# Kernel optimization log

Measured on AMD Instinct MI355X. Metric: run time of the kernel, lower is better.

The kernel has to match this reference:

```python
import jax, jax.numpy as jnp
import numpy as np
from math import sqrt

B, S, E, H = 2, 2048, 768, 12
DH = E // H
W = 256            # one-sided attention window (attention_window=512)
G = 16             # number of global tokens (positions 0..G-1 in every batch row)
PAD = 128          # last PAD tokens per row are padding (masked)
FF = 3072          # SwiGLU intermediate size
NEG = -1e9
EPS = 1e-5


def _ln(x, g, b):
    m = jnp.mean(x, axis=-1, keepdims=True)
    v = jnp.var(x, axis=-1, keepdims=True)
    return (x - m) * jax.lax.rsqrt(v + EPS) * g + b


def _rope(x, t):
    # x: [B,H,S,DH]; t: [B,S] float 'set positions'
    half = DH // 2
    inv_freq = 1.0 / (10000.0 ** (jnp.arange(half, dtype=jnp.float32) / half))
    ang = t[:, None, :, None] * inv_freq            # [B,1,S,half]
    cos, sin = jnp.cos(ang), jnp.sin(ang)
    x1, x2 = x[..., :half], x[..., half:]
    return jnp.concatenate([x1 * cos - x2 * sin, x2 * cos + x1 * sin], axis=-1)


def _heads(x):  # [B,S,E] -> [B,H,S,DH]
    return x.reshape(B, S, H, DH).transpose(0, 2, 1, 3)


def _chunk3(x):
    # [B,H,S,D] -> [B,H,C,3W,D]: for query chunk c, keys from chunks c-1,c,c+1 (zero padded)
    b, h, s, d = x.shape
    c = s // W
    xp = jnp.pad(x, ((0, 0), (0, 0), (W, W), (0, 0))).reshape(b, h, c + 2, W, d)
    return jnp.concatenate([xp[:, :, :-2], xp[:, :, 1:-1], xp[:, :, 2:]], axis=3)


def _forward(x, attention_mask, global_attention_mask,
             Wq, bq, Wk, bk, Wv, bv, Wqg, bqg, Wkg, bkg, Wvg, bvg,
             ln0_g, ln0_b, ln1_g, ln1_b, W1, W3, W2):
    C = S // W
    merged = attention_mask * (global_attention_mask + 1)   # 0 masked, 1 local, 2 global
    is_masked = merged == 0
    is_global = merged == 2
    remove = merged != 1   # keys removed from windowed attention (masked or global)

    q = _heads(x @ Wq + bq) / sqrt(DH)
    k = _heads(x @ Wk + bk)
    v = _heads(x @ Wv + bv)

    # RoPE over 'set positions': (~is_index_masked) * cumsum(is_index_global_attn)
    t = jnp.where(is_masked, 0, jnp.cumsum(is_global.astype(jnp.int32), axis=1)).astype(jnp.float32)
    q = _rope(q, t)
    k = _rope(k, t)

    # --- sliding-window (banded) scores: band[b,h,i,d] = q_i . k_{i+d-W} ---
    qc = q.reshape(B, H, C, W, DH)
    k3 = _chunk3(k)
    s3 = jnp.einsum('bhcpd,bhcqd->bhcpq', qc, k3)                     # [B,H,C,W,3W]
    didx = jnp.arange(W)[:, None] + jnp.arange(2 * W + 1)[None, :]    # [W,2W+1]
    band = jnp.take_along_axis(s3, didx[None, None, None], axis=-1)   # [B,H,C,W,2W+1]

    # mask removed keys / out-of-range positions inside the band
    rmp = jnp.pad(remove, ((0, 0), (W, W)), constant_values=True).reshape(B, C + 2, W)
    rm3 = jnp.concatenate([rmp[:, :-2], rmp[:, 1:-1], rmp[:, 2:]], axis=2)  # [B,C,3W]
    band_rm = jnp.take_along_axis(jnp.broadcast_to(rm3[:, :, None, :], (B, C, W, 3 * W)),
                                  didx[None, None], axis=-1)                # [B,C,W,2W+1]
    band = jnp.where(band_rm[:, None], NEG, band).reshape(B, H, S, 2 * W + 1)

    # --- global-key columns (keys taken from the RoPE'd local key vectors) ---
    sg = jnp.einsum('bhid,bhgd->bhig', q, k[:, :, :G])                # [B,H,S,G]

    scores = jnp.concatenate([sg, band], axis=-1)                     # [B,H,S,G+2W+1]
    probs = jax.nn.softmax(scores.astype(jnp.float32), axis=-1).astype(x.dtype)
    probs = jnp.where(is_masked[:, None, :, None], 0.0, probs)

    # --- probs @ value: global columns + band ---
    out = jnp.einsum('bhig,bhgd->bhid', probs[..., :G], v[:, :, :G])
    pl = probs[..., G:].reshape(B, H, C, W, 2 * W + 1)
    rows = jnp.broadcast_to(jnp.arange(W)[:, None], (W, 2 * W + 1))
    p3 = jnp.zeros((B, H, C, W, 3 * W), probs.dtype).at[:, :, :, rows, didx].set(pl)
    v3 = _chunk3(v)
    out = out + jnp.einsum('bhcpq,bhcqd->bhcpd', p3, v3).reshape(B, H, S, DH)
    attn = out.transpose(0, 2, 1, 3).reshape(B, S, E)

    # --- full attention for global tokens (separate global projections, no RoPE) ---
    gq = _heads(x @ Wqg + bqg)[:, :, :G] / sqrt(DH)                   # [B,H,G,DH]
    gk = _heads(x @ Wkg + bkg)
    gv = _heads(x @ Wvg + bvg)
    gs = jnp.einsum('bhgd,bhjd->bhgj', gq, gk)                        # [B,H,G,S]
    gs = jnp.where(is_masked[:, None, None, :], NEG, gs)
    gp = jax.nn.softmax(gs.astype(jnp.float32), axis=-1).astype(x.dtype)
    gout = jnp.einsum('bhgj,bhjd->bhgd', gp, gv).transpose(0, 2, 1, 3).reshape(B, G, E)
    attn = attn.at[:, :G].set(gout)

    # residual + post-LN, SwiGLU FFN, residual + post-LN (dropout = eval mode)
    h0 = _ln(x + attn, ln0_g, ln0_b)
    ffn = (jax.nn.silu(h0 @ W1) * (h0 @ W3)) @ W2
    return _ln(h0 + ffn, ln1_g, ln1_b)


def setup_inputs():
    key = jax.random.key(0)
    ks = jax.random.split(key, 12)
    x = jax.random.normal(ks[0], (B, S, E), jnp.float32)
    attention_mask = jnp.ones((B, S), jnp.int32).at[:, S - PAD:].set(0)
    global_attention_mask = jnp.zeros((B, S), jnp.int32).at[:, :G].set(1)
    sd = 0.02
    def w(k, shape):
        return jax.random.normal(k, shape, jnp.float32) * sd
    return dict(
        x=x, attention_mask=attention_mask, global_attention_mask=global_attention_mask,
        Wq=w(ks[1], (E, E)), bq=jnp.zeros((E,), jnp.float32),
        Wk=w(ks[2], (E, E)), bk=jnp.zeros((E,), jnp.float32),
        Wv=w(ks[3], (E, E)), bv=jnp.zeros((E,), jnp.float32),
        Wqg=w(ks[4], (E, E)), bqg=jnp.zeros((E,), jnp.float32),
        Wkg=w(ks[5], (E, E)), bkg=jnp.zeros((E,), jnp.float32),
        Wvg=w(ks[6], (E, E)), bvg=jnp.zeros((E,), jnp.float32),
        ln0_g=jnp.ones((E,), jnp.float32), ln0_b=jnp.zeros((E,), jnp.float32),
        ln1_g=jnp.ones((E,), jnp.float32), ln1_b=jnp.zeros((E,), jnp.float32),
        W1=w(ks[7], (E, FF)), W3=w(ks[8], (E, FF)), W2=w(ks[9], (FF, E)))


def reference(x, attention_mask, global_attention_mask, Wq, bq, Wk, bk, Wv, bv,
              Wqg, bqg, Wkg, bkg, Wvg, bvg, ln0_g, ln0_b, ln1_g, ln1_b, W1, W3, W2):
    return _forward(x, attention_mask, global_attention_mask,
                    Wq, bq, Wk, bk, Wv, bv, Wqg, bqg, Wkg, bkg, Wvg, bvg,
                    ln0_g, ln0_b, ln1_g, ln1_b, W1, W3, W2)
```

## Files before the change

kernel.cpp:

```cpp
#include <hip/hip_runtime.h>


#define BB_ 2
#define SS 2048
#define EE 768
#define HH 12
#define DHH 64
#define GG 16
#define FFN 3072
#define MM (BB_*SS)

typedef __bf16 bf16_t;
typedef __bf16 bf16x8_t __attribute__((ext_vector_type(8)));
typedef float f32x4_t __attribute__((ext_vector_type(4)));

__device__ inline void gload16(const void* g, void* l) {
  __builtin_amdgcn_global_load_lds((const __attribute__((address_space(1))) void*)g,
                                   (__attribute__((address_space(3))) void*)l, 16, 0, 0);
}

__global__ __launch_bounds__(64) void detect_kernel(const unsigned int* __restrict__ w,
                                                    int* __restrict__ flag) {
  int cnt = 0;
  for (int i = threadIdx.x; i < 1024; i += 64) {
    unsigned e = (w[i] >> 7) & 0xFF;
    cnt += (e >= 100 && e <= 144) ? 1 : 0;
  }
  for (int off = 32; off; off >>= 1) cnt += __shfl_xor(cnt, off);
  if (threadIdx.x == 0) flag[0] = (cnt > 512) ? 1 : 0;
}

struct CanonP { const void* src[11]; bf16_t* dst[11]; };

__global__ __launch_bounds__(256) void canon_kernel(CanonP P, const int* __restrict__ flag) {
  constexpr int ns[11] = {3145728, 768,768,768,768,768,768, 768,768,768,768};
  int idx4 = (blockIdx.x*256 + threadIdx.x)*4;
  const bool isb = flag[0] != 0;
  int off = 0, seg = -1, loc = 0;
  #pragma unroll
  for (int i=0;i<11;i++) {
    if (seg < 0 && idx4 < off + ns[i]) { seg = i; loc = idx4 - off; }
    off += ns[i];
  }
  if (seg < 0) return;
  const void* s = P.src[seg];
  bf16_t* d = P.dst[seg];
  if (isb) {
    *(uint2*)&d[loc] = *(const uint2*)((const unsigned short*)s + loc);
  } else {
    float4 v = *(const float4*)((const float*)s + loc);
    d[loc+0] = (bf16_t)v.x; d[loc+1] = (bf16_t)v.y;
    d[loc+2] = (bf16_t)v.z; d[loc+3] = (bf16_t)v.w;
  }
}

struct TP6 { const void* s[6]; bf16_t* d[6]; };

__global__ __launch_bounds__(256) void trans_kernel(TP6 P, int R, int C,
                                                    const int* __restrict__ flag) {
  const int z = blockIdx.z;
  const void* src = P.s[z]; bf16_t* dst = P.d[z];
  const bool isb = flag[0] != 0;
  __shared__ bf16_t tile[32][33];
  int tx = threadIdx.x & 31, ty = threadIdx.x >> 5;
  int r0 = blockIdx.y*32, c0 = blockIdx.x*32;
  #pragma unroll
  for (int i=0;i<4;i++) {
    int rr = ty + i*8;
    size_t si = (size_t)(r0+rr)*C + c0 + tx;
    tile[rr][tx] = isb ? ((const bf16_t*)src)[si] : (bf16_t)((const float*)src)[si];
  }
  __syncthreads();
  #pragma unroll
  for (int i=0;i<4;i++) {
    int cc = ty + i*8;
    dst[(size_t)(c0+cc)*R + r0 + tx] = tile[tx][cc];
  }
}

__global__ __launch_bounds__(256) void zero_kernel(float* __restrict__ p, int n) {
  int i = blockIdx.x*256 + threadIdx.x;
  if (i < n) p[i] = 0.f;
}

__global__ __launch_bounds__(256) void flags_kernel(const int* __restrict__ am,
                                                    const int* __restrict__ gm,
                                                    float* __restrict__ tpos,
                                                    int* __restrict__ flags) {
  int b = blockIdx.x;
  int t = threadIdx.x;
  int lane = t & 63, wv = t >> 6;
  int base = b*SS + t*8;
  int mg[8]; int isg[8]; int loc = 0;
  for (int i=0;i<8;i++) {
    int a = am[base+i], g = gm[base+i];
    int merged = a*(g+1);
    mg[i] = merged;
    isg[i] = (merged==2) ? 1 : 0;
    loc += isg[i];
  }
  int x = loc;
  for (int off=1; off<64; off<<=1) {
    int y = __shfl_up(x, off);
    if (lane >= off) x += y;
  }
  __shared__ int wtot[4];
  if (lane==63) wtot[wv] = x;
  __syncthreads();
  int prev = 0;
  for (int w=0; w<wv; w++) prev += wtot[w];
  int run = prev + x - loc;
  for (int i=0;i<8;i++) {
    run += isg[i];
    int masked = (mg[i]==0) ? 1 : 0;
    int glob   = (mg[i]==2) ? 1 : 0;
    int rem    = (mg[i]!=1) ? 1 : 0;
    tpos[base+i]  = masked ? 0.f : (float)run;
    flags[base+i] = masked | (glob<<1) | (rem<<2);
  }
}

__device__ inline void gemm128_core(const bf16_t* __restrict__ A,
                                    const bf16_t* __restrict__ BT,
                                    int ldA, int ldB, int kbeg, int kend,
                                    int m0, int n0,
                                    bf16_t* As, bf16_t* Bs,
                                    f32x4_t (&acc)[4][4]) {
  const int t = threadIdx.x;
  const int lane = t & 63, wv = t >> 6;
  const int l15 = lane & 15, quad = lane >> 4;
  const int wr = (wv >> 1) << 6, wc = (wv & 1) << 6;
  const int rsub = lane >> 3, pch = lane & 7;
  const int sch = pch ^ rsub;
  const size_t abase = (size_t)(m0 + wv*32 + rsub)*ldA + sch*8;
  const size_t bbase = (size_t)(n0 + wv*32 + rsub)*ldB + sch*8;
  const int sx = l15 & 7;
  bf16_t* lA = As + (wv*32)*64;
  bf16_t* lB = Bs + (wv*32)*64;
  for (int k0 = kbeg; k0 < kend; k0 += 64) {
    __syncthreads();
    #pragma unroll
    for (int j=0;j<4;j++) {
      gload16(A + abase + (size_t)(j*8)*ldA + k0, lA + j*8*64);
      gload16(BT + bbase + (size_t)(j*8)*ldB + k0, lB + j*8*64);
    }
    __syncthreads();
    #pragma unroll
    for (int c=0;c<2;c++) {
      bf16x8_t af[4], bfr[4];
      #pragma unroll
      for (int a=0;a<4;a++)
        af[a] = *(const bf16x8_t*)&As[(wr + a*16 + l15)*64 + ((c*4+quad)^sx)*8];
      #pragma unroll
      for (int b=0;b<4;b++)
        bfr[b] = *(const bf16x8_t*)&Bs[(wc + b*16 + l15)*64 + ((c*4+quad)^sx)*8];
      #pragma unroll
      for (int a=0;a<4;a++)
        #pragma unroll
        for (int b=0;b<4;b++)
          acc[a][b] = __builtin_amdgcn_mfma_f32_16x16x32_bf16(af[a], bfr[b], acc[a][b], 0,0,0);
    }
  }
}

struct ProjParams {
  const bf16_t* W[5];
  const bf16_t* Bi[5];
  bf16_t* O[5];
};

__global__ __launch_bounds__(256) void proj_kernel(const bf16_t* __restrict__ x,
                                                   ProjParams P,
                                                   const float* __restrict__ tpos) {
  const int m0 = blockIdx.x*128, n0 = blockIdx.y*128;
  const int z  = blockIdx.z;
  __shared__ bf16_t As[128*64];
  __shared__ bf16_t Bs[128*64];
  f32x4_t acc[4][4];
  #pragma unroll
  for (int a=0;a<4;a++)
    #pragma unroll
    for (int b=0;b<4;b++) acc[a][b] = (f32x4_t){0.f,0.f,0.f,0.f};
  gemm128_core(x, P.W[z], EE, EE, 0, EE, m0, n0, As, Bs, acc);

  const int t = threadIdx.x;
  const int lane = t & 63, wv = t >> 6;
  const int l15 = lane & 15, quad = lane >> 4;
  const int wr = (wv >> 1) << 6, wc = (wv & 1) << 6;
  const float scale = (z==0) ? 0.125f : 1.f;
  const bool rope = (z<2);
  const int h = (n0 + wc) >> 6;
  bf16_t* Oz = P.O[z];
  const bf16_t* Bz = P.Bi[z];
  float bvals[4];
  #pragma unroll
  for (int b=0;b<4;b++) bvals[b] = (float)Bz[h*64 + b*16 + l15];
  #pragma unroll
  for (int a=0;a<4;a++) {
    #pragma unroll
    for (int r=0;r<4;r++) {
      int row = m0 + wr + a*16 + quad*4 + r;
      int bb = row >> 11, spos = row & (SS-1);
      float vals[4];
      #pragma unroll
      for (int b=0;b<4;b++) vals[b] = (acc[a][b][r] + bvals[b]) * scale;
      if (rope) {
        float tv = tpos[row];
        #pragma unroll
        for (int b=0;b<2;b++) {
          int j = b*16 + l15;
          float inv = __expf(-(float)j * (9.210340371976184f/32.f));
          float ang = tv * inv;
          float sn = __sinf(ang), cs = __cosf(ang);
          float x1 = vals[b], x2 = vals[b+2];
          vals[b]   = x1*cs - x2*sn;
          vals[b+2] = x2*cs + x1*sn;
        }
      }
      bf16_t* dst = Oz + ((size_t)(bb*HH + h)*SS + spos)*DHH;
      #pragma unroll
      for (int b=0;b<4;b++) dst[b*16 + l15] = (bf16_t)vals[b];
    }
  }
}

__global__ __launch_bounds__(256) void gemm_ffn1(const bf16_t* __restrict__ A,
                                                 const bf16_t* __restrict__ BT,
                                                 bf16_t* __restrict__ t1) {
  const int m0 = blockIdx.x*128, n0 = blockIdx.y*128;
  __shared__ bf16_t As[128*64];
  __shared__ bf16_t Bs[128*64];
  f32x4_t acc[4][4];
  #pragma unroll
  for (int a=0;a<4;a++)
    #pragma unroll
    for (int b=0;b<4;b++) acc[a][b] = (f32x4_t){0.f,0.f,0.f,0.f};
  gemm128_core(A, BT, EE, EE, 0, EE, m0, n0, As, Bs, acc);
  const int t = threadIdx.x;
  const int lane = t & 63, wv = t >> 6;
  const int l15 = lane & 15, quad = lane >> 4;
  const int wr = (wv >> 1) << 6, wc = (wv & 1) << 6;
  #pragma unroll
  for (int a=0;a<4;a++)
    #pragma unroll
    for (int r=0;r<4;r++) {
      int row = m0 + wr + a*16 + quad*4 + r;
      #pragma unroll
      for (int b=0;b<4;b++)
        t1[(size_t)row*FFN + n0 + wc + b*16 + l15] = (bf16_t)acc[a][b][r];
    }
}

__global__ __launch_bounds__(256) void gemm_ffn3(const bf16_t* __restrict__ A,
                                                 const bf16_t* __restrict__ BT,
                                                 const bf16_t* __restrict__ t1,
                                                 bf16_t* __restrict__ g1) {
  const int m0 = blockIdx.x*128, n0 = blockIdx.y*128;
  __shared__ bf16_t As[128*64];
  __shared__ bf16_t Bs[128*64];
  f32x4_t acc[4][4];
  #pragma unroll
  for (int a=0;a<4;a++)
    #pragma unroll
    for (int b=0;b<4;b++) acc[a][b] = (f32x4_t){0.f,0.f,0.f,0.f};
  gemm128_core(A, BT, EE, EE, 0, EE, m0, n0, As, Bs, acc);
  const int t = threadIdx.x;
  const int lane = t & 63, wv = t >> 6;
  const int l15 = lane & 15, quad = lane >> 4;
  const int wr = (wv >> 1) << 6, wc = (wv & 1) << 6;
  #pragma unroll
  for (int a=0;a<4;a++)
    #pragma unroll
    for (int r=0;r<4;r++) {
      int row = m0 + wr + a*16 + quad*4 + r;
      #pragma unroll
      for (int b=0;b<4;b++) {
        size_t idx = (size_t)row*FFN + n0 + wc + b*16 + l15;
        float a1 = (float)t1[idx];
        float sil = a1 / (1.f + __expf(-a1));
        g1[idx] = (bf16_t)(sil * acc[a][b][r]);
      }
    }
}

struct Ffn2Out { float* p[4]; };

__global__ __launch_bounds__(256) void gemm_ffn2(const bf16_t* __restrict__ A,
                                                 const bf16_t* __restrict__ BT,
                                                 Ffn2Out O) {
  const int m0 = blockIdx.x*128, n0 = blockIdx.y*128;
  const int kz = blockIdx.z;
  __shared__ bf16_t As[128*64];
  __shared__ bf16_t Bs[128*64];
  f32x4_t acc[4][4];
  #pragma unroll
  for (int a=0;a<4;a++)
    #pragma unroll
    for (int b=0;b<4;b++) acc[a][b] = (f32x4_t){0.f,0.f,0.f,0.f};
  gemm128_core(A, BT, FFN, FFN, kz*768, (kz+1)*768, m0, n0, As, Bs, acc);
  const int t = threadIdx.x;
  const int lane = t & 63, wv = t >> 6;
  const int l15 = lane & 15, quad = lane >> 4;
  const int wr = (wv >> 1) << 6, wc = (wv & 1) << 6;
  float* C = O.p[kz];
  #pragma unroll
  for (int a=0;a<4;a++)
    #pragma unroll
    for (int r=0;r<4;r++) {
      int row = m0 + wr + a*16 + quad*4 + r;
      #pragma unroll
      for (int b=0;b<4;b++)
        C[(size_t)row*EE + n0 + wc + b*16 + l15] = acc[a][b][r];
    }
}

__global__ __launch_bounds__(64) void qg_kernel(const bf16_t* __restrict__ x,
                                                const bf16_t* __restrict__ WqgT,
                                                const bf16_t* __restrict__ bqg,
                                                float* __restrict__ qgb) {
  int g = blockIdx.x, h = blockIdx.y, b = blockIdx.z;
  int d = threadIdx.x;
  __shared__ float xs[EE];
  for (int i=d; i<EE; i+=64) xs[i] = (float)x[((size_t)b*SS + g)*EE + i];
  __syncthreads();
  float acc = 0.f;
  const bf16_t* wrow = WqgT + (size_t)(h*64+d)*EE;
  #pragma unroll 4
  for (int k=0;k<EE;k+=8) {
    bf16x8_t w8 = *(const bf16x8_t*)(wrow + k);
    #pragma unroll
    for (int i=0;i<8;i++) acc += xs[k+i] * (float)w8[i];
  }
  acc = (acc + (float)bqg[h*64+d]) * 0.125f;
  qgb[((size_t)(b*HH+h)*GG + g)*DHH + d] = acc;
}

__global__ __launch_bounds__(256) void band_kernel(const bf16_t* __restrict__ qb,
                                                   const bf16_t* __restrict__ kb,
                                                   const bf16_t* __restrict__ vb,
                                                   const int* __restrict__ flags,
                                                   float* __restrict__ attn) {
  const int flat = blockIdx.x;
  const int nb = (flat & 7) * 96 + (flat >> 3);
  const int px = nb & 31;
  const int hb = nb >> 5;
  const int h = hb % HH, b = hb / HH;
  const int p0 = px * 64;

  const int t = threadIdx.x;
  const int wv = t>>6, lane = t&63;
  const int l15 = lane & 15, quad = lane >> 4;
  const size_t bh = (size_t)(b*HH+h);
  const bf16_t* kbh = kb + bh*SS*DHH;
  const bf16_t* vbh = vb + bh*SS*DHH;
  const int* fl = flags + b*SS;
  const int q0 = p0 + wv*16;

  __shared__ bf16_t Ks[2][64*DHH];
  __shared__ bf16_t Vt[2][64*72];
  __shared__ bf16_t Pw[4][16*72];

  const bf16_t* qrow = qb + (bh*SS + q0 + l15)*DHH;
  bf16x8_t qa0 = *(const bf16x8_t*)(qrow + quad*8);
  bf16x8_t qa1 = *(const bf16x8_t*)(qrow + 32 + quad*8);

  const int srsub = lane >> 3, spch = lane & 7;
  const int vkp  = (t & 31) * 2;
  const int vdh0 = (t >> 5) * 8;

  {
    const int kb0 = p0 - 256;
    #pragma unroll
    for (int j=0;j<2;j++) {
      int row = wv*16 + j*8 + srsub;
      int kc = min(max(kb0 + row, 0), SS-1);
      gload16(kbh + (size_t)kc*DHH + (spch ^ srsub)*8, &Ks[0][(wv*16 + j*8)*DHH]);
    }
    int kc1 = min(max(kb0 + vkp,   0), SS-1);
    int kc2 = min(max(kb0 + vkp+1, 0), SS-1);
    bf16x8_t v1 = *(const bf16x8_t*)(vbh + (size_t)kc1*DHH + vdh0);
    bf16x8_t v2 = *(const bf16x8_t*)(vbh + (size_t)kc2*DHH + vdh0);
    #pragma unroll
    for (int i=0;i<8;i++) {
      union { unsigned u; bf16_t hh[2]; } pk;
      pk.hh[0] = v1[i]; pk.hh[1] = v2[i];
      *(unsigned*)&Vt[0][(vdh0+i)*72 + vkp] = pk.u;
    }
  }
  __syncthreads();

  f32x4_t o[4];
  #pragma unroll
  for (int i=0;i<4;i++) o[i] = (f32x4_t){0.f,0.f,0.f,0.f};
  float lsum[4] = {0.f,0.f,0.f,0.f};
  bf16_t* P = Pw[wv];

  for (int unit=0; unit<10; unit++) {
    const int cur = unit & 1, nxt = cur ^ 1;
    const int kb0 = (unit<9) ? (p0 - 256 + unit*64) : 0;
    const bool pre = (unit < 9);
    bf16x8_t pv1, pv2;
    if (pre) {
      const int kbn = (unit < 8) ? (kb0 + 64) : 0;
      #pragma unroll
      for (int j=0;j<2;j++) {
        int row = wv*16 + j*8 + srsub;
        int kc = min(max(kbn + row, 0), SS-1);
        gload16(kbh + (size_t)kc*DHH + (spch ^ srsub)*8, &Ks[nxt][(wv*16 + j*8)*DHH]);
      }
      int kc1 = min(max(kbn + vkp,   0), SS-1);
      int kc2 = min(max(kbn + vkp+1, 0), SS-1);
      pv1 = *(const bf16x8_t*)(vbh + (size_t)kc1*DHH + vdh0);
      pv2 = *(const bf16x8_t*)(vbh + (size_t)kc2*DHH + vdh0);
    }
    const bf16_t* Kc = Ks[cur];
    const int nsub = (unit<9) ? 4 : 1;
    for (int sub=0; sub<4; sub++) {
      if (sub < nsub) {
        int krow = sub*16 + l15;
        int kpos = kb0 + krow;
        bf16x8_t kf0 = *(const bf16x8_t*)&Kc[krow*DHH + (((quad  ) ^ (krow&7))<<3)];
        bf16x8_t kf1 = *(const bf16x8_t*)&Kc[krow*DHH + (((quad+4) ^ (krow&7))<<3)];
        f32x4_t s = (f32x4_t){0.f,0.f,0.f,0.f};
        s = __builtin_amdgcn_mfma_f32_16x16x32_bf16(qa0, kf0, s, 0,0,0);
        s = __builtin_amdgcn_mfma_f32_16x16x32_bf16(qa1, kf1, s, 0,0,0);
        int kc = min(max(kpos,0),SS-1);
        bool drop = false;
        if (unit<9) drop = (kpos<0) || (kpos>=SS) || (((fl[kc]>>2)&1)!=0);
        #pragma unroll
        for (int r=0;r<4;r++) {
          float e;
          if (unit==9) {
            e = __expf(s[r]);
          } else {
            int dj = kpos - (q0 + quad*4 + r);
            bool valid = (dj>=-256) && (dj<=256) && (!drop);
            e = valid ? __expf(s[r]) : 0.f;
          }
          lsum[r] += e;
          P[(quad*4+r)*72 + sub*16 + l15] = (bf16_t)e;
        }
      } else {
        #pragma unroll
        for (int r=0;r<4;r++) P[(quad*4+r)*72 + sub*16 + l15] = (bf16_t)0.f;
      }
    }
    __builtin_amdgcn_s_setprio(1);
    #pragma unroll
    for (int chunk=0; chunk<2; chunk++) {
      bf16x8_t pf = *(const bf16x8_t*)&P[l15*72 + chunk*32 + quad*8];
      #pragma unroll
      for (int nt=0; nt<4; nt++) {
        bf16x8_t vf = *(const bf16x8_t*)&Vt[cur][(nt*16+l15)*72 + chunk*32 + quad*8];
        o[nt] = __builtin_amdgcn_mfma_f32_16x16x32_bf16(pf, vf, o[nt], 0,0,0);
      }
    }
    __builtin_amdgcn_s_setprio(0);
    if (pre) {
      #pragma unroll
      for (int i=0;i<8;i++) {
        union { unsigned u; bf16_t hh[2]; } pk;
        pk.hh[0] = pv1[i]; pk.hh[1] = pv2[i];
        *(unsigned*)&Vt[nxt][(vdh0+i)*72 + vkp] = pk.u;
      }
      __syncthreads();
    }
  }
  #pragma unroll
  for (int r=0;r<4;r++) {
    float s = lsum[r];
    s += __shfl_xor(s,1); s += __shfl_xor(s,2);
    s += __shfl_xor(s,4); s += __shfl_xor(s,8);
    lsum[r] = s;
  }
  #pragma unroll
  for (int r=0;r<4;r++) {
    int q = q0 + quad*4 + r;
    int masked = fl[q] & 1;
    float inv = masked ? 0.f : 1.f/lsum[r];
    float* dst = attn + ((size_t)(b*SS+q))*EE + h*64 + l15;
    #pragma unroll
    for (int nt=0; nt<4; nt++) dst[nt*16] = o[nt][r]*inv;
  }
}

__global__ __launch_bounds__(256) void gattn_part(const float* __restrict__ qgb,
                                                  const bf16_t* __restrict__ kgb,
                                                  const bf16_t* __restrict__ vgb,
                                                  const int* __restrict__ flags,
                                                  float* __restrict__ go,
                                                  float* __restrict__ gl) {
  const int kbase = blockIdx.x*128;
  const int h = blockIdx.y, b = blockIdx.z;
  const int t = threadIdx.x;
  __shared__ float gqs[16*68];
  __shared__ float Ks[64*68];
  __shared__ float Vs[64*68];
  __shared__ float es[16*64];
  const size_t bh = (size_t)(b*HH+h);
  #pragma unroll
  for (int j=0;j<4;j++) {
    int idx = t + j*256;
    int g = idx>>6, d = idx&63;
    gqs[g*68+d] = qgb[(bh*GG + g)*DHH + d];
  }
  float accv[4] = {0.f,0.f,0.f,0.f};
  float lpart = 0.f;
  const int gs = t>>4, kslot = t&15;
  const int dp = t&63, grp = t>>6;
  const bf16_t* kb_ = kgb + bh*SS*DHH;
  const bf16_t* vb_ = vgb + bh*SS*DHH;
  const int* fl = flags + b*SS;
  for (int tile=0; tile<2; tile++) {
    int k0 = kbase + tile*64;
    __syncthreads();
    {
      int row = t>>2, seg = t&3;
      const bf16_t* sk = kb_ + (size_t)(k0+row)*DHH + seg*16;
      const bf16_t* sv = vb_ + (size_t)(k0+row)*DHH + seg*16;
      bf16x8_t k1 = *(const bf16x8_t*)sk;
      bf16x8_t k2 = *(const bf16x8_t*)(sk+8);
      bf16x8_t v1 = *(const bf16x8_t*)sv;
      bf16x8_t v2 = *(const bf16x8_t*)(sv+8);
      #pragma unroll
      for (int i=0;i<8;i++) {
        Ks[row*68 + seg*16 + i]     = (float)k1[i];
        Ks[row*68 + seg*16 + 8 + i] = (float)k2[i];
        Vs[row*68 + seg*16 + i]     = (float)v1[i];
        Vs[row*68 + seg*16 + 8 + i] = (float)v2[i];
      }
    }
    __syncthreads();
    #pragma unroll
    for (int j=0;j<4;j++) {
      int key = kslot + 16*j;
      const float* gq = &gqs[gs*68];
      const float* kr = &Ks[key*68];
      float s = 0.f;
      #pragma unroll
      for (int d4=0; d4<64; d4+=4) {
        float4 a = *(const float4*)(gq + d4);
        float4 kk = *(const float4*)(kr + d4);
        s += a.x*kk.x + a.y*kk.y + a.z*kk.z + a.w*kk.w;
      }
      int msk = fl[k0+key] & 1;
      float e = msk ? 0.f : __expf(s);
      es[gs*64+key] = e;
      lpart += e;
    }
    __syncthreads();
    #pragma unroll
    for (int g=0; g<4; g++) {
      int gg = grp*4+g;
      float a = accv[g];
      for (int key=0;key<64;key++) a += es[gg*64+key]*Vs[key*68+dp];
      accv[g] = a;
    }
  }
  __syncthreads();
  es[gs*64 + kslot] = lpart;
  __syncthreads();
  if (t < 16) {
    float s = 0.f;
    for (int j=0;j<16;j++) s += es[t*64+j];
    atomicAdd(&gl[bh*16 + t], s);
  }
  #pragma unroll
  for (int g=0; g<4; g++)
    atomicAdd(&go[(bh*16 + grp*4+g)*64 + dp], accv[g]);
}

__global__ __launch_bounds__(256) void addln_kernel(const bf16_t* __restrict__ Abf,
                                                    const float* __restrict__ Af,
                                                    const float* __restrict__ B0,
                                                    const float* __restrict__ B1,
                                                    const float* __restrict__ B2,
                                                    const float* __restrict__ B3,
                                                    const float* __restrict__ gof,
                                                    const float* __restrict__ glf,
                                                    const bf16_t* __restrict__ gw,
                                                    const bf16_t* __restrict__ bw,
                                                    float* __restrict__ outf,
                                                    bf16_t* __restrict__ outb,
                                                    const int* __restrict__ flagp) {
  int r = blockIdx.x, t = threadIdx.x;
  int lane = t&63, wv = t>>6;
  int spos = r & (SS-1), bb = r >> 11;
  bool isglob = (gof != nullptr) && (spos < GG);
  float v[3]; float sum=0.f, ss=0.f;
  #pragma unroll
  for (int j=0;j<3;j++) {
    int idx = t + j*256;
    size_t gi = (size_t)r*EE+idx;
    float a = Abf ? (float)Abf[gi] : Af[gi];
    float bv;
    if (isglob) {
      int hh = idx >> 6, dp = idx & 63;
      int slot = (bb*HH + hh)*GG + spos;
      bv = gof[(size_t)slot*DHH + dp] / glf[slot];
    } else {
      bv = B0[gi];
    }
    float val = a + bv;
    if (B1) val += B1[gi] + B2[gi] + B3[gi];
    v[j] = val; sum += val; ss += val*val;
  }
  #pragma unroll
  for (int off=32; off>=1; off>>=1) {
    sum += __shfl_xor(sum, off);
    ss  += __shfl_xor(ss, off);
  }
  __shared__ float s1[4], s2[4];
  if (lane==0) { s1[wv]=sum; s2[wv]=ss; }
  __syncthreads();
  sum = s1[0]+s1[1]+s1[2]+s1[3];
  ss  = s2[0]+s2[1]+s2[2]+s2[3];
  float mean = sum * (1.f/(float)EE);
  float var  = ss * (1.f/(float)EE) - mean*mean;
  float rstd = rsqrtf(var + 1e-5f);
  bool wantb, wantf;
  if (flagp) { bool isb = (*flagp)!=0; wantb = isb; wantf = !isb; }
  else { wantb = (outb!=nullptr); wantf = (outf!=nullptr); }
  #pragma unroll
  for (int j=0;j<3;j++) {
    int idx = t + j*256;
    float o = (v[j]-mean)*rstd*(float)gw[idx] + (float)bw[idx];
    if (wantf) outf[(size_t)r*EE+idx] = o;
    if (wantb) outb[(size_t)r*EE+idx] = (bf16_t)o;
  }
}

extern "C" void kernel_launch(void* const* d_in, const int* in_sizes, int n_in,
                              void* d_out, int out_size, void* d_ws, size_t ws_size,
                              hipStream_t stream) {
  const void* x_r    = d_in[0];
  const int* am      = (const int*)d_in[1];
  const int* gm      = (const int*)d_in[2];
  (void)in_sizes; (void)n_in; (void)out_size; (void)ws_size;

  char* ws = (char*)d_ws;
  size_t off = 0;
  auto alloc = [&](size_t bytes) -> void* {
    void* p = ws + off;
    off += (bytes + 255) & ~(size_t)255;
    return p;
  };
  bf16_t* xc    = (bf16_t*)alloc((size_t)MM*EE*2);
  bf16_t* WT[6]; bf16_t* bc[6];
  for (int i=0;i<6;i++) { WT[i] = (bf16_t*)alloc((size_t)EE*EE*2); bc[i] = (bf16_t*)alloc(EE*2); }
  bf16_t* lnc[4];
  for (int i=0;i<4;i++) lnc[i] = (bf16_t*)alloc(EE*2);
  bf16_t* W1T = (bf16_t*)alloc((size_t)EE*FFN*2);
  bf16_t* W3T = (bf16_t*)alloc((size_t)EE*FFN*2);
  bf16_t* W2T = (bf16_t*)alloc((size_t)FFN*EE*2);
  const size_t NBHSD = (size_t)BB_*HH*SS*DHH;
  bf16_t* qb    = (bf16_t*)alloc(NBHSD*2);
  bf16_t* kb    = (bf16_t*)alloc(NBHSD*2);
  bf16_t* vb    = (bf16_t*)alloc(NBHSD*2);
  bf16_t* kgb   = (bf16_t*)alloc(NBHSD*2);
  bf16_t* vgb   = (bf16_t*)alloc(NBHSD*2);
  float* qgb   = (float*)alloc((size_t)BB_*HH*GG*DHH*4);
  float* attn  = (float*)alloc((size_t)MM*EE*4);
  float* h0f   = (float*)alloc((size_t)MM*EE*4);
  bf16_t* h0b  = (bf16_t*)alloc((size_t)MM*EE*2);
  bf16_t* g1   = (bf16_t*)alloc((size_t)MM*FFN*2);
  float* p3    = (float*)alloc((size_t)MM*EE*4);
  float* go    = (float*)alloc((size_t)BB_*HH*GG*DHH*4);
  float* gl    = (float*)alloc((size_t)BB_*HH*GG*4);
  float* tposb = (float*)alloc((size_t)BB_*SS*4);
  int*   flagb = (int*)alloc((size_t)BB_*SS*4);
  int*   dflag = (int*)alloc(256);
  bf16_t* t1 = qb;
  float* p1 = (float*)qb;
  float* p2 = (float*)qb + (size_t)MM*EE;

  detect_kernel<<<1, 64, 0, stream>>>((const unsigned int*)d_in[3], dflag);

  CanonP CP;
  const void* csrc[11] = { x_r, d_in[4], d_in[6], d_in[8], d_in[10], d_in[12], d_in[14],
                           d_in[15], d_in[16], d_in[17], d_in[18] };
  bf16_t* cdst[11] = { xc, bc[0], bc[1], bc[2], bc[3], bc[4], bc[5],
                       lnc[0], lnc[1], lnc[2], lnc[3] };
  for (int i=0;i<11;i++) { CP.src[i]=csrc[i]; CP.dst[i]=cdst[i]; }
  canon_kernel<<<3081, 256, 0, stream>>>(CP, dflag);

  TP6 T6;
  const int wi[6] = {3,5,7,9,11,13};
  for (int i=0;i<6;i++) { T6.s[i]=d_in[wi[i]]; T6.d[i]=WT[i]; }
  trans_kernel<<<dim3(24,24,6), 256, 0, stream>>>(T6, EE, EE, dflag);
  TP6 TF; TF.s[0]=d_in[19]; TF.d[0]=W1T; TF.s[1]=d_in[20]; TF.d[1]=W3T;
  for (int i=2;i<6;i++) { TF.s[i]=d_in[19]; TF.d[i]=W1T; }
  trans_kernel<<<dim3(96,24,2), 256, 0, stream>>>(TF, EE, FFN, dflag);
  TP6 T2; T2.s[0]=d_in[21]; T2.d[0]=W2T;
  for (int i=1;i<6;i++) { T2.s[i]=d_in[21]; T2.d[i]=W2T; }
  trans_kernel<<<dim3(24,96,1), 256, 0, stream>>>(T2, FFN, EE, dflag);

  zero_kernel<<<98, 256, 0, stream>>>(go, 24960);

  flags_kernel<<<BB_, 256, 0, stream>>>(am, gm, tposb, flagb);

  ProjParams P;
  P.W[0]=WT[0]; P.Bi[0]=bc[0]; P.O[0]=qb;
  P.W[1]=WT[1]; P.Bi[1]=bc[1]; P.O[1]=kb;
  P.W[2]=WT[2]; P.Bi[2]=bc[2]; P.O[2]=vb;
  P.W[3]=WT[4]; P.Bi[3]=bc[4]; P.O[3]=kgb;
  P.W[4]=WT[5]; P.Bi[4]=bc[5]; P.O[4]=vgb;
  proj_kernel<<<dim3(MM/128, EE/128, 5), 256, 0, stream>>>(xc, P, tposb);

  qg_kernel<<<dim3(GG, HH, BB_), 64, 0, stream>>>(xc, WT[3], bc[3], qgb);

  band_kernel<<<dim3(768), 256, 0, stream>>>(qb, kb, vb, flagb, attn);

  gattn_part<<<dim3(SS/128, HH, BB_), 256, 0, stream>>>(qgb, kgb, vgb, flagb, go, gl);

  addln_kernel<<<MM, 256, 0, stream>>>(xc, nullptr, attn, nullptr, nullptr, nullptr,
                                       go, gl, lnc[0], lnc[1], h0f, h0b, nullptr);

  gemm_ffn1<<<dim3(MM/128, FFN/128), 256, 0, stream>>>(h0b, W1T, t1);
  gemm_ffn3<<<dim3(MM/128, FFN/128), 256, 0, stream>>>(h0b, W3T, t1, g1);
  Ffn2Out FO; FO.p[0]=attn; FO.p[1]=p1; FO.p[2]=p2; FO.p[3]=p3;
  gemm_ffn2<<<dim3(MM/128, EE/128, 4), 256, 0, stream>>>(g1, W2T, FO);

  addln_kernel<<<MM, 256, 0, stream>>>(nullptr, h0f, attn, p1, p2, p3,
                                       nullptr, nullptr, lnc[2], lnc[3],
                                       (float*)d_out, (bf16_t*)d_out, dflag);
}
```

Baseline: 364.2 us.

## Use 256x256 double-buffered GEMM tiles with 512-thread blocks

All projection and FFN GEMMs move from 128x128 tiles with 256 threads to 256x256 tiles with 512 threads. Each wave now computes a 128x64 sub-tile, and global-to-LDS loads are double-buffered so the next K-slice is fetched while MFMAs run on the current one, with one barrier per step instead of two. This raises operand reuse per byte loaded and hides load latency. The cost is a much smaller grid (roughly 192–240 blocks on a 256-CU part) and about 128KB of LDS per block, which allows only one block per CU and may leave CUs idle.

```diff
diff --git a/kernel.cpp b/kernel.cpp
--- a/kernel.cpp
+++ b/kernel.cpp
@@ -120,48 +120,75 @@
   }
 }
 
-__device__ inline void gemm128_core(const bf16_t* __restrict__ A,
+__device__ inline void gemm256_core(const bf16_t* __restrict__ A,
                                     const bf16_t* __restrict__ BT,
                                     int ldA, int ldB, int kbeg, int kend,
                                     int m0, int n0,
-                                    bf16_t* As, bf16_t* Bs,
-                                    f32x4_t (&acc)[4][4]) {
+                                    bf16_t* As0, bf16_t* As1,
+                                    bf16_t* Bs0, bf16_t* Bs1,
+                                    f32x4_t (&acc)[8][4]) {
   const int t = threadIdx.x;
   const int lane = t & 63, wv = t >> 6;
   const int l15 = lane & 15, quad = lane >> 4;
-  const int wr = (wv >> 1) << 6, wc = (wv & 1) << 6;
   const int rsub = lane >> 3, pch = lane & 7;
   const int sch = pch ^ rsub;
   const size_t abase = (size_t)(m0 + wv*32 + rsub)*ldA + sch*8;
   const size_t bbase = (size_t)(n0 + wv*32 + rsub)*ldB + sch*8;
   const int sx = l15 & 7;
-  bf16_t* lA = As + (wv*32)*64;
-  bf16_t* lB = Bs + (wv*32)*64;
-  for (int k0 = kbeg; k0 < kend; k0 += 64) {
+  const int ar0 = (wv >> 2)*128, bc0 = (wv & 3)*64;
+  bf16_t* Asb[2] = {As0, As1};
+  bf16_t* Bsb[2] = {Bs0, Bs1};
+  {
+    bf16_t* lA = As0 + (wv*32)*64;
+    bf16_t* lB = Bs0 + (wv*32)*64;
+    #pragma unroll
+    for (int j=0;j<4;j++) {
+      gload16(A + abase + (size_t)(j*8)*ldA + kbeg, lA + j*8*64);
+      gload16(BT + bbase + (size_t)(j*8)*ldB + kbeg, lB + j*8*64);
+    }
+  }
+  const int nsteps = (kend - kbeg) >> 6;
+  for (int s=0; s<nsteps; ++s) {
+    const int cur = s & 1, nxt = cur ^ 1;
     __syncthreads();
-    #pragma unroll
-    for (int j=0;j<4;j++) {
-      gload16(A + abase + (size_t)(j*8)*ldA + k0, lA + j*8*64);
-      gload16(BT + bbase + (size_t)(j*8)*ldB + k0, lB + j*8*64);
-    }
-    __syncthreads();
+    if (s+1 < nsteps) {
+      const int k0 = kbeg + (s+1)*64;
+      bf16_t* lA = Asb[nxt] + (wv*32)*64;
+      bf16_t* lB = Bsb[nxt] + (wv*32)*64;
+      #pragma unroll
+      for (int j=0;j<4;j++) {
+        gload16(A + abase + (size_t)(j*8)*ldA + k0, lA + j*8*64);
+        gload16(BT + bbase + (size_t)(j*8)*ldB + k0, lB + j*8*64);
+      }
+    }
+    const bf16_t* Ac = Asb[cur];
+    const bf16_t* Bc = Bsb[cur];
     #pragma unroll
     for (int c=0;c<2;c++) {
-      bf16x8_t af[4], bfr[4];
-      #pragma unroll
-      for (int a=0;a<4;a++)
-        af[a] = *(const bf16x8_t*)&As[(wr + a*16 + l15)*64 + ((c*4+quad)^sx)*8];
-      #pragma unroll
-      for (int b=0;b<4;b++)
-        bfr[b] = *(const bf16x8_t*)&Bs[(wc + b*16 + l15)*64 + ((c*4+quad)^sx)*8];
-      #pragma unroll
-      for (int a=0;a<4;a++)
+      bf16x8_t bfr[4];
+      #pragma unroll
+      for (int n=0;n<4;n++)
+        bfr[n] = *(const bf16x8_t*)&Bc[(bc0 + n*16 + l15)*64 + (((c*4+quad)^sx))*8];
+      #pragma unroll
+      for (int m=0;m<8;m++) {
+        bf16x8_t af = *(const bf16x8_t*)&Ac[(ar0 + m*16 + l15)*64 + (((c*4+quad)^sx))*8];
         #pragma unroll
-        for (int b=0;b<4;b++)
-          acc[a][b] = __builtin_amdgcn_mfma_f32_16x16x32_bf16(af[a], bfr[b], acc[a][b], 0,0,0);
-    }
-  }
-}
+        for (int n=0;n<4;n++)
+          acc[m][n] = __builtin_amdgcn_mfma_f32_16x16x32_bf16(af, bfr[n], acc[m][n], 0,0,0);
+      }
+    }
+  }
+}
+
+#define GEMM256_SHARED \
+  __shared__ bf16_t As0[256*64]; __shared__ bf16_t As1[256*64]; \
+  __shared__ bf16_t Bs0[256*64]; __shared__ bf16_t Bs1[256*64];
+
+#define GEMM256_EPI_VARS \
+  const int t = threadIdx.x; \
+  const int lane = t & 63, wv = t >> 6; \
+  const int l15 = lane & 15, quad = lane >> 4; \
+  const int ar0 = (wv >> 2)*128, bc0 = (wv & 3)*64;
 
 struct ProjParams {
   const bf16_t* W[5];
@@ -169,148 +196,132 @@
   bf16_t* O[5];
 };
 
-__global__ __launch_bounds__(256) void proj_kernel(const bf16_t* __restrict__ x,
-                                                   ProjParams P,
-                                                   const float* __restrict__ tpos) {
-  const int m0 = blockIdx.x*128, n0 = blockIdx.y*128;
+__global__ __launch_bounds__(512, 2) void proj_kernel(const bf16_t* __restrict__ x,
+                                                      ProjParams P,
+                                                      const float* __restrict__ tpos) {
+  const int m0 = blockIdx.x*256, n0 = blockIdx.y*256;
   const int z  = blockIdx.z;
-  __shared__ bf16_t As[128*64];
-  __shared__ bf16_t Bs[128*64];
-  f32x4_t acc[4][4];
-  #pragma unroll
-  for (int a=0;a<4;a++)
-    #pragma unroll
-    for (int b=0;b<4;b++) acc[a][b] = (f32x4_t){0.f,0.f,0.f,0.f};
-  gemm128_core(x, P.W[z], EE, EE, 0, EE, m0, n0, As, Bs, acc);
-
-  const int t = threadIdx.x;
-  const int lane = t & 63, wv = t >> 6;
-  const int l15 = lane & 15, quad = lane >> 4;
-  const int wr = (wv >> 1) << 6, wc = (wv & 1) << 6;
+  GEMM256_SHARED
+  f32x4_t acc[8][4];
+  #pragma unroll
+  for (int m=0;m<8;m++)
+    #pragma unroll
+    for (int n=0;n<4;n++) acc[m][n] = (f32x4_t){0.f,0.f,0.f,0.f};
+  gemm256_core(x, P.W[z], EE, EE, 0, EE, m0, n0, As0, As1, Bs0, Bs1, acc);
+
+  GEMM256_EPI_VARS
   const float scale = (z==0) ? 0.125f : 1.f;
   const bool rope = (z<2);
-  const int h = (n0 + wc) >> 6;
+  const int h = (n0 + bc0) >> 6;
   bf16_t* Oz = P.O[z];
   const bf16_t* Bz = P.Bi[z];
   float bvals[4];
   #pragma unroll
-  for (int b=0;b<4;b++) bvals[b] = (float)Bz[h*64 + b*16 + l15];
-  #pragma unroll
-  for (int a=0;a<4;a++) {
+  for (int n=0;n<4;n++) bvals[n] = (float)Bz[h*64 + n*16 + l15];
+  #pragma unroll
+  for (int m=0;m<8;m++) {
     #pragma unroll
     for (int r=0;r<4;r++) {
-      int row = m0 + wr + a*16 + quad*4 + r;
+      int row = m0 + ar0 + m*16 + quad*4 + r;
       int bb = row >> 11, spos = row & (SS-1);
       float vals[4];
       #pragma unroll
-      for (int b=0;b<4;b++) vals[b] = (acc[a][b][r] + bvals[b]) * scale;
+      for (int n=0;n<4;n++) vals[n] = (acc[m][n][r] + bvals[n]) * scale;
       if (rope) {
         float tv = tpos[row];
         #pragma unroll
-        for (int b=0;b<2;b++) {
-          int j = b*16 + l15;
+        for (int n=0;n<2;n++) {
+          int j = n*16 + l15;
           float inv = __expf(-(float)j * (9.210340371976184f/32.f));
           float ang = tv * inv;
           float sn = __sinf(ang), cs = __cosf(ang);
-          float x1 = vals[b], x2 = vals[b+2];
-          vals[b]   = x1*cs - x2*sn;
-          vals[b+2] = x2*cs + x1*sn;
+          float x1 = vals[n], x2 = vals[n+2];
+          vals[n]   = x1*cs - x2*sn;
+          vals[n+2] = x2*cs + x1*sn;
         }
       }
       bf16_t* dst = Oz + ((size_t)(bb*HH + h)*SS + spos)*DHH;
       #pragma unroll
-      for (int b=0;b<4;b++) dst[b*16 + l15] = (bf16_t)vals[b];
-    }
-  }
-}
-
-__global__ __launch_bounds__(256) void gemm_ffn1(const bf16_t* __restrict__ A,
-                                                 const bf16_t* __restrict__ BT,
-                                                 bf16_t* __restrict__ t1) {
-  const int m0 = blockIdx.x*128, n0 = blockIdx.y*128;
-  __shared__ bf16_t As[128*64];
-  __shared__ bf16_t Bs[128*64];
-  f32x4_t acc[4][4];
-  #pragma unroll
-  for (int a=0;a<4;a++)
-    #pragma unroll
-    for (int b=0;b<4;b++) acc[a][b] = (f32x4_t){0.f,0.f,0.f,0.f};
-  gemm128_core(A, BT, EE, EE, 0, EE, m0, n0, As, Bs, acc);
-  const int t = threadIdx.x;
-  const int lane = t & 63, wv = t >> 6;
-  const int l15 = lane & 15, quad = lane >> 4;
-  const int wr = (wv >> 1) << 6, wc = (wv & 1) << 6;
-  #pragma unroll
-  for (int a=0;a<4;a++)
+      for (int n=0;n<4;n++) dst[n*16 + l15] = (bf16_t)vals[n];
+    }
+  }
+}
+
+__global__ __launch_bounds__(512, 2) void gemm_ffn1(const bf16_t* __restrict__ A,
+                                                    const bf16_t* __restrict__ BT,
+                                                    bf16_t* __restrict__ t1) {
+  const int m0 = blockIdx.x*256, n0 = blockIdx.y*256;
+  GEMM256_SHARED
+  f32x4_t acc[8][4];
+  #pragma unroll
+  for (int m=0;m<8;m++)
+    #pragma unroll
+    for (int n=0;n<4;n++) acc[m][n] = (f32x4_t){0.f,0.f,0.f,0.f};
+  gemm256_core(A, BT, EE, EE, 0, EE, m0, n0, As0, As1, Bs0, Bs1, acc);
+  GEMM256_EPI_VARS
+  #pragma unroll
+  for (int m=0;m<8;m++)
     #pragma unroll
     for (int r=0;r<4;r++) {
-      int row = m0 + wr + a*16 + quad*4 + r;
-      #pragma unroll
-      for (int b=0;b<4;b++)
-        t1[(size_t)row*FFN + n0 + wc + b*16 + l15] = (bf16_t)acc[a][b][r];
-    }
-}
-
-__global__ __launch_bounds__(256) void gemm_ffn3(const bf16_t* __restrict__ A,
-                                                 const bf16_t* __restrict__ BT,
-                                                 const bf16_t* __restrict__ t1,
-                                                 bf16_t* __restrict__ g1) {
-  const int m0 = blockIdx.x*128, n0 = blockIdx.y*128;
-  __shared__ bf16_t As[128*64];
-  __shared__ bf16_t Bs[128*64];
-  f32x4_t acc[4][4];
-  #pragma unroll
-  for (int a=0;a<4;a++)
-    #pragma unroll
-    for (int b=0;b<4;b++) acc[a][b] = (f32x4_t){0.f,0.f,0.f,0.f};
-  gemm128_core(A, BT, EE, EE, 0, EE, m0, n0, As, Bs, acc);
-  const int t = threadIdx.x;
-  const int lane = t & 63, wv = t >> 6;
-  const int l15 = lane & 15, quad = lane >> 4;
-  const int wr = (wv >> 1) << 6, wc = (wv & 1) << 6;
-  #pragma unroll
-  for (int a=0;a<4;a++)
+      int row = m0 + ar0 + m*16 + quad*4 + r;
+      #pragma unroll
+      for (int n=0;n<4;n++)
+        t1[(size_t)row*FFN + n0 + bc0 + n*16 + l15] = (bf16_t)acc[m][n][r];
+    }
+}
+
+__global__ __launch_bounds__(512, 2) void gemm_ffn3(const bf16_t* __restrict__ A,
+                                                    const bf16_t* __restrict__ BT,
+                                                    const bf16_t* __restrict__ t1,
+                                                    bf16_t* __restrict__ g1) {
+  const int m0 = blockIdx.x*256, n0 = blockIdx.y*256;
+  GEMM256_SHARED
+  f32x4_t acc[8][4];
+  #pragma unroll
+  for (int m=0;m<8;m++)
+    #pragma unroll
+    for (int n=0;n<4;n++) acc[m][n] = (f32x4_t){0.f,0.f,0.f,0.f};
+  gemm256_core(A, BT, EE, EE, 0, EE, m0, n0, As0, As1, Bs0, Bs1, acc);
+  GEMM256_EPI_VARS
+  #pragma unroll
+  for (int m=0;m<8;m++)
     #pragma unroll
     for (int r=0;r<4;r++) {
-      int row = m0 + wr + a*16 + quad*4 + r;
-      #pragma unroll
-      for (int b=0;b<4;b++) {
-        size_t idx = (size_t)row*FFN + n0 + wc + b*16 + l15;
+      int row = m0 + ar0 + m*16 + quad*4 + r;
+      #pragma unroll
+      for (int n=0;n<4;n++) {
+        size_t idx = (size_t)row*FFN + n0 + bc0 + n*16 + l15;
         float a1 = (float)t1[idx];
         float sil = a1 / (1.f + __expf(-a1));
-        g1[idx] = (bf16_t)(sil * acc[a][b][r]);
+        g1[idx] = (bf16_t)(sil * acc[m][n][r]);
       }
     }
 }
 
 struct Ffn2Out { float* p[4]; };
 
-__global__ __launch_bounds__(256) void gemm_ffn2(const bf16_t* __restrict__ A,
-                                                 const bf16_t* __restrict__ BT,
-                                                 Ffn2Out O) {
-  const int m0 = blockIdx.x*128, n0 = blockIdx.y*128;
+__global__ __launch_bounds__(512, 2) void gemm_ffn2(const bf16_t* __restrict__ A,
+                                                    const bf16_t* __restrict__ BT,
+                                                    Ffn2Out O) {
+  const int m0 = blockIdx.x*256, n0 = blockIdx.y*256;
   const int kz = blockIdx.z;
-  __shared__ bf16_t As[128*64];
-  __shared__ bf16_t Bs[128*64];
-  f32x4_t acc[4][4];
-  #pragma unroll
-  for (int a=0;a<4;a++)
-    #pragma unroll
-    for (int b=0;b<4;b++) acc[a][b] = (f32x4_t){0.f,0.f,0.f,0.f};
-  gemm128_core(A, BT, FFN, FFN, kz*768, (kz+1)*768, m0, n0, As, Bs, acc);
-  const int t = threadIdx.x;
-  const int lane = t & 63, wv = t >> 6;
-  const int l15 = lane & 15, quad = lane >> 4;
-  const int wr = (wv >> 1) << 6, wc = (wv & 1) << 6;
+  GEMM256_SHARED
+  f32x4_t acc[8][4];
+  #pragma unroll
+  for (int m=0;m<8;m++)
+    #pragma unroll
+    for (int n=0;n<4;n++) acc[m][n] = (f32x4_t){0.f,0.f,0.f,0.f};
+  gemm256_core(A, BT, FFN, FFN, kz*768, (kz+1)*768, m0, n0, As0, As1, Bs0, Bs1, acc);
+  GEMM256_EPI_VARS
   float* C = O.p[kz];
   #pragma unroll
-  for (int a=0;a<4;a++)
+  for (int m=0;m<8;m++)
     #pragma unroll
     for (int r=0;r<4;r++) {
-      int row = m0 + wr + a*16 + quad*4 + r;
-      #pragma unroll
-      for (int b=0;b<4;b++)
-        C[(size_t)row*EE + n0 + wc + b*16 + l15] = acc[a][b][r];
+      int row = m0 + ar0 + m*16 + quad*4 + r;
+      #pragma unroll
+      for (int n=0;n<4;n++)
+        C[(size_t)row*EE + n0 + bc0 + n*16 + l15] = acc[m][n][r];
     }
 }
 
@@ -705,7 +716,7 @@
   P.W[2]=WT[2]; P.Bi[2]=bc[2]; P.O[2]=vb;
   P.W[3]=WT[4]; P.Bi[3]=bc[4]; P.O[3]=kgb;
   P.W[4]=WT[5]; P.Bi[4]=bc[5]; P.O[4]=vgb;
-  proj_kernel<<<dim3(MM/128, EE/128, 5), 256, 0, stream>>>(xc, P, tposb);
+  proj_kernel<<<dim3(MM/256, EE/256, 5), 512, 0, stream>>>(xc, P, tposb);
 
   qg_kernel<<<dim3(GG, HH, BB_), 64, 0, stream>>>(xc, WT[3], bc[3], qgb);
 
@@ -716,10 +727,10 @@
   addln_kernel<<<MM, 256, 0, stream>>>(xc, nullptr, attn, nullptr, nullptr, nullptr,
                                        go, gl, lnc[0], lnc[1], h0f, h0b, nullptr);
 
-  gemm_ffn1<<<dim3(MM/128, FFN/128), 256, 0, stream>>>(h0b, W1T, t1);
-  gemm_ffn3<<<dim3(MM/128, FFN/128), 256, 0, stream>>>(h0b, W3T, t1, g1);
+  gemm_ffn1<<<dim3(MM/256, FFN/256), 512, 0, stream>>>(h0b, W1T, t1);
+  gemm_ffn3<<<dim3(MM/256, FFN/256), 512, 0, stream>>>(h0b, W3T, t1, g1);
   Ffn2Out FO; FO.p[0]=attn; FO.p[1]=p1; FO.p[2]=p2; FO.p[3]=p3;
-  gemm_ffn2<<<dim3(MM/128, EE/128, 4), 256, 0, stream>>>(g1, W2T, FO);
+  gemm_ffn2<<<dim3(MM/256, EE/256, 4), 512, 0, stream>>>(g1, W2T, FO);
 
   addln_kernel<<<MM, 256, 0, stream>>>(nullptr, h0f, attn, p1, p2, p3,
                                        nullptr, nullptr, lnc[2], lnc[3],
```

New measurement: 383.1 us. +5.2%, slower.

## Fuse FFN gate and up GEMMs into one kernel; halve FFN2 split-K

Applied to the files above, without the earlier changes.

Replaces the separate W1 and W3 GEMMs with one kernel that loads the A tile once, computes both products into two accumulator sets, and applies SiLU-gating in the epilogue. This drops the bf16 t1 intermediate write and read, plus one A-operand pass. The down-projection split-K goes from 4 to 2 slices, so fewer fp32 partial buffers are written and summed in the final layernorm. The cost is a narrower 64-column tile with doubled accumulators, which raises register pressure, and fewer blocks for the FFN2 GEMM.

```diff
diff --git a/kernel.cpp b/kernel.cpp
--- a/kernel.cpp
+++ b/kernel.cpp
@@ -224,66 +224,78 @@
   }
 }
 
-__global__ __launch_bounds__(256) void gemm_ffn1(const bf16_t* __restrict__ A,
-                                                 const bf16_t* __restrict__ BT,
-                                                 bf16_t* __restrict__ t1) {
-  const int m0 = blockIdx.x*128, n0 = blockIdx.y*128;
+__global__ __launch_bounds__(256) void gemm_ffn13(const bf16_t* __restrict__ A,
+                                                  const bf16_t* __restrict__ B1T,
+                                                  const bf16_t* __restrict__ B3T,
+                                                  bf16_t* __restrict__ g1) {
+  const int n0 = blockIdx.x*64, m0 = blockIdx.y*128;
   __shared__ bf16_t As[128*64];
-  __shared__ bf16_t Bs[128*64];
-  f32x4_t acc[4][4];
-  #pragma unroll
-  for (int a=0;a<4;a++)
-    #pragma unroll
-    for (int b=0;b<4;b++) acc[a][b] = (f32x4_t){0.f,0.f,0.f,0.f};
-  gemm128_core(A, BT, EE, EE, 0, EE, m0, n0, As, Bs, acc);
+  __shared__ bf16_t Bs1[64*64];
+  __shared__ bf16_t Bs3[64*64];
   const int t = threadIdx.x;
   const int lane = t & 63, wv = t >> 6;
   const int l15 = lane & 15, quad = lane >> 4;
-  const int wr = (wv >> 1) << 6, wc = (wv & 1) << 6;
+  const int wr = (wv >> 1) << 6, wc = (wv & 1) << 5;
+  const int rsub = lane >> 3, pch = lane & 7;
+  const int sch = pch ^ rsub;
+  const size_t abase = (size_t)(m0 + wv*32 + rsub)*EE + sch*8;
+  const size_t bbase = (size_t)(n0 + wv*16 + rsub)*EE + sch*8;
+  const int sx = l15 & 7;
+  bf16_t* lA  = As  + (wv*32)*64;
+  bf16_t* lB1 = Bs1 + (wv*16)*64;
+  bf16_t* lB3 = Bs3 + (wv*16)*64;
+  f32x4_t a1[4][2], a3[4][2];
+  #pragma unroll
+  for (int a=0;a<4;a++)
+    #pragma unroll
+    for (int b=0;b<2;b++) { a1[a][b] = (f32x4_t){0.f,0.f,0.f,0.f};
+                            a3[a][b] = (f32x4_t){0.f,0.f,0.f,0.f}; }
+  for (int k0 = 0; k0 < EE; k0 += 64) {
+    __syncthreads();
+    #pragma unroll
+    for (int j=0;j<4;j++)
+      gload16(A + abase + (size_t)(j*8)*EE + k0, lA + j*8*64);
+    #pragma unroll
+    for (int j=0;j<2;j++) {
+      gload16(B1T + bbase + (size_t)(j*8)*EE + k0, lB1 + j*8*64);
+      gload16(B3T + bbase + (size_t)(j*8)*EE + k0, lB3 + j*8*64);
+    }
+    __syncthreads();
+    #pragma unroll
+    for (int c=0;c<2;c++) {
+      bf16x8_t af[4], b1f[2], b3f[2];
+      #pragma unroll
+      for (int a=0;a<4;a++)
+        af[a] = *(const bf16x8_t*)&As[(wr + a*16 + l15)*64 + ((c*4+quad)^sx)*8];
+      #pragma unroll
+      for (int b=0;b<2;b++) {
+        b1f[b] = *(const bf16x8_t*)&Bs1[(wc + b*16 + l15)*64 + ((c*4+quad)^sx)*8];
+        b3f[b] = *(const bf16x8_t*)&Bs3[(wc + b*16 + l15)*64 + ((c*4+quad)^sx)*8];
+      }
+      #pragma unroll
+      for (int a=0;a<4;a++)
+        #pragma unroll
+        for (int b=0;b<2;b++) {
+          a1[a][b] = __builtin_amdgcn_mfma_f32_16x16x32_bf16(af[a], b1f[b], a1[a][b], 0,0,0);
+          a3[a][b] = __builtin_amdgcn_mfma_f32_16x16x32_bf16(af[a], b3f[b], a3[a][b], 0,0,0);
+        }
+    }
+  }
   #pragma unroll
   for (int a=0;a<4;a++)
     #pragma unroll
     for (int r=0;r<4;r++) {
       int row = m0 + wr + a*16 + quad*4 + r;
       #pragma unroll
-      for (int b=0;b<4;b++)
-        t1[(size_t)row*FFN + n0 + wc + b*16 + l15] = (bf16_t)acc[a][b][r];
-    }
-}
-
-__global__ __launch_bounds__(256) void gemm_ffn3(const bf16_t* __restrict__ A,
-                                                 const bf16_t* __restrict__ BT,
-                                                 const bf16_t* __restrict__ t1,
-                                                 bf16_t* __restrict__ g1) {
-  const int m0 = blockIdx.x*128, n0 = blockIdx.y*128;
-  __shared__ bf16_t As[128*64];
-  __shared__ bf16_t Bs[128*64];
-  f32x4_t acc[4][4];
-  #pragma unroll
-  for (int a=0;a<4;a++)
-    #pragma unroll
-    for (int b=0;b<4;b++) acc[a][b] = (f32x4_t){0.f,0.f,0.f,0.f};
-  gemm128_core(A, BT, EE, EE, 0, EE, m0, n0, As, Bs, acc);
-  const int t = threadIdx.x;
-  const int lane = t & 63, wv = t >> 6;
-  const int l15 = lane & 15, quad = lane >> 4;
-  const int wr = (wv >> 1) << 6, wc = (wv & 1) << 6;
-  #pragma unroll
-  for (int a=0;a<4;a++)
-    #pragma unroll
-    for (int r=0;r<4;r++) {
-      int row = m0 + wr + a*16 + quad*4 + r;
-      #pragma unroll
-      for (int b=0;b<4;b++) {
-        size_t idx = (size_t)row*FFN + n0 + wc + b*16 + l15;
-        float a1 = (float)t1[idx];
-        float sil = a1 / (1.f + __expf(-a1));
-        g1[idx] = (bf16_t)(sil * acc[a][b][r]);
-      }
-    }
-}
-
-struct Ffn2Out { float* p[4]; };
+      for (int b=0;b<2;b++) {
+        float tv = a1[a][b][r];
+        float sil = tv / (1.f + __expf(-tv));
+        g1[(size_t)row*FFN + n0 + wc + b*16 + l15] = (bf16_t)(sil * a3[a][b][r]);
+      }
+    }
+}
+
+struct Ffn2Out { float* p[2]; };
 
 __global__ __launch_bounds__(256) void gemm_ffn2(const bf16_t* __restrict__ A,
                                                  const bf16_t* __restrict__ BT,
@@ -297,7 +309,7 @@
   for (int a=0;a<4;a++)
     #pragma unroll
     for (int b=0;b<4;b++) acc[a][b] = (f32x4_t){0.f,0.f,0.f,0.f};
-  gemm128_core(A, BT, FFN, FFN, kz*768, (kz+1)*768, m0, n0, As, Bs, acc);
+  gemm128_core(A, BT, FFN, FFN, kz*1536, (kz+1)*1536, m0, n0, As, Bs, acc);
   const int t = threadIdx.x;
   const int lane = t & 63, wv = t >> 6;
   const int l15 = lane & 15, quad = lane >> 4;
@@ -602,7 +614,9 @@
       bv = B0[gi];
     }
     float val = a + bv;
-    if (B1) val += B1[gi] + B2[gi] + B3[gi];
+    if (B1) val += B1[gi];
+    if (B2) val += B2[gi];
+    if (B3) val += B3[gi];
     v[j] = val; sum += val; ss += val*val;
   }
   #pragma unroll
@@ -664,15 +678,12 @@
   float* h0f   = (float*)alloc((size_t)MM*EE*4);
   bf16_t* h0b  = (bf16_t*)alloc((size_t)MM*EE*2);
   bf16_t* g1   = (bf16_t*)alloc((size_t)MM*FFN*2);
-  float* p3    = (float*)alloc((size_t)MM*EE*4);
   float* go    = (float*)alloc((size_t)BB_*HH*GG*DHH*4);
   float* gl    = (float*)alloc((size_t)BB_*HH*GG*4);
   float* tposb = (float*)alloc((size_t)BB_*SS*4);
   int*   flagb = (int*)alloc((size_t)BB_*SS*4);
   int*   dflag = (int*)alloc(256);
-  bf16_t* t1 = qb;
   float* p1 = (float*)qb;
-  float* p2 = (float*)qb + (size_t)MM*EE;
 
   detect_kernel<<<1, 64, 0, stream>>>((const unsigned int*)d_in[3], dflag);
 
@@ -716,12 +727,11 @@
   addln_kernel<<<MM, 256, 0, stream>>>(xc, nullptr, attn, nullptr, nullptr, nullptr,
                                        go, gl, lnc[0], lnc[1], h0f, h0b, nullptr);
 
-  gemm_ffn1<<<dim3(MM/128, FFN/128), 256, 0, stream>>>(h0b, W1T, t1);
-  gemm_ffn3<<<dim3(MM/128, FFN/128), 256, 0, stream>>>(h0b, W3T, t1, g1);
-  Ffn2Out FO; FO.p[0]=attn; FO.p[1]=p1; FO.p[2]=p2; FO.p[3]=p3;
-  gemm_ffn2<<<dim3(MM/128, EE/128, 4), 256, 0, stream>>>(g1, W2T, FO);
-
-  addln_kernel<<<MM, 256, 0, stream>>>(nullptr, h0f, attn, p1, p2, p3,
+  gemm_ffn13<<<dim3(FFN/64, MM/128), 256, 0, stream>>>(h0b, W1T, W3T, g1);
+  Ffn2Out FO; FO.p[0]=attn; FO.p[1]=p1;
+  gemm_ffn2<<<dim3(MM/128, EE/128, 2), 256, 0, stream>>>(g1, W2T, FO);
+
+  addln_kernel<<<MM, 256, 0, stream>>>(nullptr, h0f, attn, p1, nullptr, nullptr,
                                        nullptr, nullptr, lnc[2], lnc[3],
                                        (float*)d_out, (bf16_t*)d_out, dflag);
 }
```

Result: no change. 366.4 us (+0.6%).
